# Performance work log

Hardware: AMD Instinct MI355X
Metric: run time of the kernel (lower is better)

## Reference

```python
import jax, jax.numpy as jnp
import numpy as np


@jax.custom_vjp
def binary_act(x):
    # sign forward, straight-through (clipped) backward, matching BinaryActivation
    return jnp.sign(x)

def _ba_fwd(x):
    return jnp.sign(x), x

def _ba_bwd(x, g):
    return (jnp.where((x >= -1.0) & (x <= 1.0), g, 0.0),)

binary_act.defvjp(_ba_fwd, _ba_bwd)


def conv2d(x, w, b, pad, groups):
    # x: NCHW, w: OIHW
    y = jax.lax.conv_general_dilated(
        x, w, window_strides=(1, 1), padding=[(pad, pad), (pad, pad)],
        feature_group_count=groups,
        dimension_numbers=("NCHW", "OIHW", "NCHW"))
    return y + b[None, :, None, None]


def bconv(x, w, b, pad, groups):
    # Binary_conv2d: weights and bias binarized via sign (no STE on weights in torch either)
    return conv2d(x, jnp.sign(w), jnp.sign(b), pad, groups)


def maxpool2(x):
    return jax.lax.reduce_window(x, -jnp.inf, jax.lax.max,
                                 (1, 1, 2, 2), (1, 1, 2, 2), "VALID")


def setup_inputs() -> dict:
    key = jax.random.key(0)
    ks = jax.random.split(key, 14)
    d = {}
    d["x"] = jax.random.normal(ks[0], (1024, 3, 32, 32), dtype=jnp.float32)
    # conv1: depthwise 3x3 (groups=3) then 1x1 3->128
    d["w1_dw"] = jax.random.normal(ks[1], (3, 1, 3, 3), dtype=jnp.float32) * 0.1
    d["b1_dw"] = jax.random.normal(ks[2], (3,), dtype=jnp.float32) * 0.1
    d["w1_pw"] = jax.random.normal(ks[3], (128, 3, 1, 1), dtype=jnp.float32) * 0.1
    d["b1_pw"] = jax.random.normal(ks[4], (128,), dtype=jnp.float32) * 0.1
    # conv2: depthwise 3x3 (groups=128) then 1x1 128->256
    d["w2_dw"] = jax.random.normal(ks[5], (128, 1, 3, 3), dtype=jnp.float32) * 0.1
    d["b2_dw"] = jax.random.normal(ks[6], (128,), dtype=jnp.float32) * 0.1
    d["w2_pw"] = jax.random.normal(ks[7], (256, 128, 1, 1), dtype=jnp.float32) * 0.1
    d["b2_pw"] = jax.random.normal(ks[8], (256,), dtype=jnp.float32) * 0.1
    # fc layers (full precision weights, sign applied to fc1 output only)
    d["fc1_w"] = jax.random.normal(ks[9], (1024, 256 * 8 * 8), dtype=jnp.float32) * (1.0 / np.sqrt(256 * 8 * 8))
    d["fc1_b"] = jnp.zeros((1024,), dtype=jnp.float32)
    d["fc2_w"] = jax.random.normal(ks[10], (10, 1024), dtype=jnp.float32) * (1.0 / np.sqrt(1024.0))
    d["fc2_b"] = jnp.zeros((10,), dtype=jnp.float32)
    return d


def reference(x, w1_dw, b1_dw, w1_pw, b1_pw, w2_dw, b2_dw, w2_pw, b2_pw,
              fc1_w, fc1_b, fc2_w, fc2_b):
    h = bconv(x, w1_dw, b1_dw, pad=1, groups=3)        # [B,3,32,32]
    h = bconv(h, w1_pw, b1_pw, pad=0, groups=1)        # [B,128,32,32]
    h = maxpool2(binary_act(h))                        # [B,128,16,16]
    h = bconv(h, w2_dw, b2_dw, pad=1, groups=128)      # [B,128,16,16]
    h = bconv(h, w2_pw, b2_pw, pad=0, groups=1)        # [B,256,16,16]
    h = maxpool2(binary_act(h))                        # [B,256,8,8]
    h = h.reshape(h.shape[0], -1)                      # [B,16384]
    h = binary_act(h @ fc1_w.T + fc1_b)                # [B,1024]
    return h @ fc2_w.T + fc2_b                         # [B,10]
```

## Files before the change

### kernel.cpp

```cpp
#include <hip/hip_runtime.h>


__device__ __forceinline__ int fsign(float v)  { return (v > 0.f) - (v < 0.f); }
__device__ __forceinline__ int dsign(double v) { return (v > 0.0) - (v < 0.0); }

typedef int v4i __attribute__((ext_vector_type(4)));

__device__ __forceinline__ void async16(const signed char* g, signed char* l) {
    __builtin_amdgcn_global_load_lds(
        (const __attribute__((address_space(1))) void*)g,
        (__attribute__((address_space(3))) void*)l, 16, 0, 0);
}

__global__ void k1_conv1(const float* __restrict__ x,
                         const float* __restrict__ w1dw, const float* __restrict__ b1dw,
                         const float* __restrict__ w1pw, const float* __restrict__ b1pw,
                         const float* __restrict__ w2pw, const float* __restrict__ b2pw,
                         signed char* __restrict__ pooled1T,
                         signed char* __restrict__ w2s, int* __restrict__ b2adj)
{
    __shared__ float sdw[27], sbdw[3];
    __shared__ unsigned char spidx[128];
    __shared__ __align__(16) signed char Obuf[32768];
    int t = threadIdx.x;
    if (t < 27) sdw[t] = (float)fsign(w1dw[t]);
    if (t < 3)  sbdw[t] = (float)fsign(b1dw[t]);
    if (t < 128) {
        int b0 = w1pw[t * 3 + 0] > 0.f;
        int b1 = w1pw[t * 3 + 1] > 0.f;
        int b2 = w1pw[t * 3 + 2] > 0.f;
        int b3 = b1pw[t] > 0.f;
        spidx[t] = (unsigned char)(b0 | (b1 << 1) | (b2 << 2) | (b3 << 3));
    }
    __syncthreads();

    int g  = blockIdx.x * 256 + t;
    int px = g & 15, py = (g >> 4) & 15, n = g >> 8;

    double h[3][4];
    const float* xb = x + (size_t)n * 3 * 1024;
    #pragma unroll
    for (int c = 0; c < 3; c++) {
        const float* xc = xb + c * 1024;
        #pragma unroll
        for (int dy = 0; dy < 2; dy++)
        #pragma unroll
        for (int dx = 0; dx < 2; dx++) {
            int y = 2 * py + dy, xx = 2 * px + dx;
            double acc = (double)sbdw[c];
            #pragma unroll
            for (int ky = 0; ky < 3; ky++) {
                int yy = y + ky - 1;
                if (yy < 0 || yy > 31) continue;
                #pragma unroll
                for (int kx = 0; kx < 3; kx++) {
                    int xxx = xx + kx - 1;
                    if (xxx < 0 || xxx > 31) continue;
                    acc += (double)sdw[c * 9 + ky * 3 + kx] * (double)xc[yy * 32 + xxx];
                }
            }
            h[c][dy * 2 + dx] = acc;
        }
    }

    double tv[4][4];
    #pragma unroll
    for (int q = 0; q < 4; q++) {
        double u = h[0][q] + h[1][q];
        double v = h[0][q] - h[1][q];
        tv[0][q] = v - h[2][q];
        tv[1][q] = u - h[2][q];
        tv[2][q] = v + h[2][q];
        tv[3][q] = u + h[2][q];
    }
    int mpack = 0;
    #pragma unroll
    for (int bp = 0; bp < 4; bp++) {
        int mxP = -2, mnP = 2, mxM = -2, mnM = 2;
        #pragma unroll
        for (int q = 0; q < 4; q++) {
            int sP = dsign(tv[bp][q] + 1.0);
            int sM = dsign(tv[bp][q] - 1.0);
            mxP = max(mxP, sP); mnP = min(mnP, sP);
            mxM = max(mxM, sM); mnM = min(mnM, sM);
        }
        int pat1 = 1 | (bp << 1);
        int pat0 = (~pat1) & 7;
        mpack |= (mxP + 1)   << (2 * (pat1 | 8));
        mpack |= (mxM + 1)   << (2 * pat1);
        mpack |= ((-mnM) + 1) << (2 * (pat0 | 8));
        mpack |= ((-mnP) + 1) << (2 * pat0);
    }

    signed char* orow = Obuf + t * 128;
    const int* pint = (const int*)spidx;
    for (int ob = 0; ob < 32; ob++) {
        int pw = pint[ob];
        int cur = 0;
        #pragma unroll
        for (int e = 0; e < 4; e++) {
            int pi = (pw >> (8 * e)) & 15;
            int mv = ((mpack >> (pi * 2)) & 3) - 1;
            cur |= (mv & 0xff) << (8 * e);
        }
        int ad = (((ob >> 2) ^ (t & 7)) << 4) + (ob & 3) * 4;
        *(int*)(orow + ad) = cur;
    }
    __syncthreads();

    signed char* outb = pooled1T + (size_t)blockIdx.x * 32768;
    #pragma unroll
    for (int r = 0; r < 8; r++) {
        int o = r * 4096 + t * 16;
        int pix = o >> 7, gg = (o >> 4) & 7;
        *(int4*)(outb + o) = *(const int4*)&Obuf[pix * 128 + ((gg ^ (pix & 7)) << 4)];
    }

    if (blockIdx.x == 0) {
        int o = t;
        int rs = 0;
        for (int cq = 0; cq < 32; cq++) {
            float4 w = *(const float4*)(w2pw + (size_t)o * 128 + cq * 4);
            int s0 = fsign(w.x), s1 = fsign(w.y), s2 = fsign(w.z), s3 = fsign(w.w);
            rs += s0 + s1 + s2 + s3;
            int pk = (s0 & 0xff) | ((s1 & 0xff) << 8) | ((s2 & 0xff) << 16) | ((s3 & 0xff) << 24);
            *(int*)(w2s + (size_t)o * 128 + cq * 4) = pk;
        }
        b2adj[o] = fsign(b2pw[o]) - 32 * rs;
    }
}

__global__ __launch_bounds__(256, 4) void k3_fused(
    const signed char* __restrict__ pooled1T,
    const float* __restrict__ w2dw, const float* __restrict__ b2dw,
    const signed char* __restrict__ w2s, const int* __restrict__ b2adj,
    signed char* __restrict__ hT2)
{
    __shared__ __align__(16) signed char Ps[32768];
    __shared__ __align__(16) signed char Uni[5120];
    __shared__ int sb2adj[256];

    signed char* sw4  = Uni;
    signed char* sdb2 = Uni + 1152;
    signed char* Os   = Uni;

    int t = threadIdx.x, l = t & 63, wid = t >> 6;
    int n = blockIdx.x;
    const signed char* pb = pooled1T + (size_t)n * 32768;

    #pragma unroll
    for (int it = 0; it < 8; it++) {
        int off = it * 4096 + t * 16;
        int p = off >> 7, seg = (off >> 4) & 7;
        *(int4*)&Ps[p * 128 + ((seg ^ (p & 7)) * 16)] = *(const int4*)(pb + off);
    }
    for (int i = t; i < 1152; i += 256) {
        int c = i & 127, tap = i >> 7;
        sw4[tap * 128 + c] = (signed char)fsign(w2dw[c * 9 + tap]);
    }
    if (t < 128) sdb2[t] = (signed char)(fsign(b2dw[t]) + 1);
    if (t < 256) sb2adj[t] = b2adj[t];
    __syncthreads();

    int frow = l & 15;

    v4i af[4][2];
    #pragma unroll
    for (int ks = 0; ks < 2; ks++) {
        int c0 = ks * 64 + (l >> 4) * 16;
        int cc = c0 >> 4;
        int4 w4[9];
        #pragma unroll
        for (int tap = 0; tap < 9; tap++)
            w4[tap] = *(const int4*)&sw4[tap * 128 + c0];
        int4 sdbv = *(const int4*)&sdb2[c0];

        #pragma unroll
        for (int i = 0; i < 4; i++) {
            int r = (wid * 4 + i) * 16 + frow;
            int py = r >> 5, px2 = (r >> 2) & 7, dy = (r >> 1) & 1, dx = r & 1;
            int y = 2 * py + dy, x = 2 * px2 + dx;
            int4 cnt = (int4){0, 0, 0, 0};
            #pragma unroll
            for (int ky = 0; ky < 3; ky++) {
                int yy = y + ky - 1;
                int yc = min(max(yy, 0), 15);
                #pragma unroll
                for (int kx = 0; kx < 3; kx++) {
                    int xx2 = x + kx - 1;
                    int xc = min(max(xx2, 0), 15);
                    int inb = ((yy == yc) && (xx2 == xc)) ? 0x01010101 : 0;
                    int p = yc * 16 + xc;
                    int4 v = *(const int4*)&Ps[p * 128 + ((cc ^ (p & 7)) * 16)];
                    int4 w = w4[ky * 3 + kx];
                    cnt.x += ((v.x ^ w.x) >> 1) & inb;
                    cnt.y += ((v.y ^ w.y) >> 1) & inb;
                    cnt.z += ((v.z ^ w.z) >> 1) & inb;
                    cnt.w += ((v.w ^ w.w) >> 1) & inb;
                }
            }
            int valid = (1 + (y > 0) + (y < 15)) * (1 + (x > 0) + (x < 15));
            int mb = (valid + 31) * 0x01010101;
            int4 u;
            u.x = sdbv.x + mb - (cnt.x + cnt.x);
            u.y = sdbv.y + mb - (cnt.y + cnt.y);
            u.z = sdbv.z + mb - (cnt.z + cnt.z);
            u.w = sdbv.w + mb - (cnt.w + cnt.w);
            af[i][ks] = (v4i){u.x, u.y, u.z, u.w};
        }
    }

    for (int oc = 0; oc < 4; oc++) {
        v4i acc[4][4];
        #pragma unroll
        for (int i = 0; i < 4; i++)
            #pragma unroll
            for (int jt = 0; jt < 4; jt++) acc[i][jt] = (v4i){0, 0, 0, 0};

        #pragma unroll
        for (int ks = 0; ks < 2; ks++) {
            v4i bf[4];
            #pragma unroll
            for (int jt = 0; jt < 4; jt++)
                bf[jt] = *(const v4i*)(w2s + (size_t)(oc * 64 + jt * 16 + frow) * 128
                                       + ks * 64 + (l >> 4) * 16);
            __builtin_amdgcn_s_setprio(1);
            #pragma unroll
            for (int i = 0; i < 4; i++)
                #pragma unroll
                for (int jt = 0; jt < 4; jt++)
                    acc[i][jt] = __builtin_amdgcn_mfma_i32_16x16x64_i8(af[i][ks], bf[jt], acc[i][jt], 0, 0, 0);
            __builtin_amdgcn_s_setprio(0);
        }

        __syncthreads();
        #pragma unroll
        for (int jt = 0; jt < 4; jt++) {
            int o_l = jt * 16 + frow;
            int bia = sb2adj[oc * 64 + o_l];
            #pragma unroll
            for (int i = 0; i < 4; i++) {
                int mx = -2;
                #pragma unroll
                for (int rr = 0; rr < 4; rr++) {
                    int p = acc[i][jt][rr] + bia;
                    int s = (p > 0) - (p < 0);
                    mx = s > mx ? s : mx;
                }
                int pp = (wid * 4 + i) * 4 + (l >> 4);
                Os[o_l * 80 + pp] = (signed char)mx;
            }
        }
        __syncthreads();
        *(int4*)&hT2[(size_t)n * 16384 + oc * 4096 + t * 16]
            = *(const int4*)&Os[(t >> 2) * 80 + (t & 3) * 16];
    }
}

__global__ void kprep(const float* __restrict__ fc1w, signed char* __restrict__ BL)
{
    int t = threadIdx.x;
    int b = blockIdx.x;
    int j = b >> 4, kb = b & 15;
    int k0 = kb * 1024 + t * 4;
    float4 w = *(const float4*)(fc1w + (size_t)j * 16384 + k0);
    float we[4] = {w.x, w.y, w.z, w.w};
    int out[4] = {0, 0, 0, 0};
    #pragma unroll
    for (int e = 0; e < 4; e++) {
        int q = (int)rint((double)we[e] * 4294967296.0);
        q = min(max(q, -266338304), 266338304);
        int d0 = ((q + 64) & 127) - 64; q = (q - d0) >> 7;
        int d1 = ((q + 64) & 127) - 64; q = (q - d1) >> 7;
        int d2 = ((q + 64) & 127) - 64; q = (q - d2) >> 7;
        int d3 = q;
        out[0] |= (d0 & 0xff) << (8 * e);
        out[1] |= (d1 & 0xff) << (8 * e);
        out[2] |= (d2 & 0xff) << (8 * e);
        out[3] |= (d3 & 0xff) << (8 * e);
    }
    #pragma unroll
    for (int m = 0; m < 4; m++)
        *(int*)(BL + (size_t)(j * 4 + m) * 16384 + k0) = out[m];
}

__global__ __launch_bounds__(512, 2) void k4a_fc1(
    const signed char* __restrict__ hT2, const signed char* __restrict__ BL,
    double* __restrict__ Pd)
{
    __shared__ __align__(16) signed char smem[98304];
    int t = threadIdx.x, l = t & 63, wid = t >> 6;
    int nb0 = blockIdx.y * 128, jb0 = blockIdx.x * 256;
    int kh = blockIdx.z, k0 = kh * 8192;
    int ksw = wid >> 2;
    int wn0 = ((wid >> 1) & 1) * 64, wj0 = (wid & 1) * 128;

    int srow = l >> 3;
    int sseg = ((l & 7) ^ srow) * 16;
    const signed char* gA = hT2 + (size_t)(nb0 + wid * 16 + srow) * 16384 + k0 + sseg;
    const signed char* gB = BL  + (size_t)(jb0 + wid * 32 + srow) * 16384 + k0 + sseg;

    v4i acc[4][8];
    #pragma unroll
    for (int i = 0; i < 4; i++)
        #pragma unroll
        for (int q = 0; q < 8; q++) acc[i][q] = (v4i){0, 0, 0, 0};

    {
        signed char* As = smem;
        signed char* Bs = smem + 16384;
        #pragma unroll
        for (int c = 0; c < 2; c++)
            async16(gA + (size_t)c * 8 * 16384, As + (wid * 16 + c * 8) * 128);
        #pragma unroll
        for (int c = 0; c < 4; c++)
            async16(gB + (size_t)c * 8 * 16384, Bs + (wid * 32 + c * 8) * 128);
    }

    int sw = (((ksw * 4) + (l >> 4)) ^ (l & 7)) * 16;

    for (int it = 0; it < 64; it++) {
        __syncthreads();
        if (it + 1 < 64) {
            int kt = (it + 1) * 128;
            signed char* As = smem + ((it + 1) & 1) * 49152;
            signed char* Bs = As + 16384;
            #pragma unroll
            for (int c = 0; c < 2; c++)
                async16(gA + (size_t)c * 8 * 16384 + kt, As + (wid * 16 + c * 8) * 128);
            #pragma unroll
            for (int c = 0; c < 4; c++)
                async16(gB + (size_t)c * 8 * 16384 + kt, Bs + (wid * 32 + c * 8) * 128);
        }
        const signed char* As = smem + (it & 1) * 49152;
        const signed char* Bs = As + 16384;
        v4i af[4], bf[8];
        #pragma unroll
        for (int i = 0; i < 4; i++)
            af[i] = *(const v4i*)&As[(wn0 + i * 16 + (l & 15)) * 128 + sw];
        #pragma unroll
        for (int q = 0; q < 8; q++)
            bf[q] = *(const v4i*)&Bs[(wj0 + q * 16 + (l & 15)) * 128 + sw];
        #pragma unroll
        for (int i = 0; i < 4; i++)
            #pragma unroll
            for (int q = 0; q < 8; q++)
                acc[i][q] = __builtin_amdgcn_mfma_i32_16x16x64_i8(af[i], bf[q], acc[i][q], 0, 0, 0);
    }

    __syncthreads();
    int* S = (int*)smem;
    #pragma unroll
    for (int h = 0; h < 2; h++) {
        if (h) __syncthreads();
        if (ksw == 0 && wn0 == h * 64) {
            #pragma unroll
            for (int i = 0; i < 4; i++)
                #pragma unroll
                for (int q = 0; q < 8; q++)
                    #pragma unroll
                    for (int rr = 0; rr < 4; rr++)
                        S[(i * 16 + (l >> 4) * 4 + rr) * 256 + (wj0 + q * 16 + (l & 15))]
                            = acc[i][q][rr];
        }
        __syncthreads();
        if (ksw == 1 && wn0 == h * 64) {
            #pragma unroll
            for (int i = 0; i < 4; i++)
                #pragma unroll
                for (int q = 0; q < 8; q++)
                    #pragma unroll
                    for (int rr = 0; rr < 4; rr++)
                        S[(i * 16 + (l >> 4) * 4 + rr) * 256 + (wj0 + q * 16 + (l & 15))]
                            += acc[i][q][rr];
        }
        __syncthreads();
        #pragma unroll
        for (int e = 0; e < 8; e++) {
            int idx = t * 8 + e;
            int n_l = idx >> 6, j_l = idx & 63;
            int4 s = *(const int4*)&S[n_l * 256 + j_l * 4];
            double val = (double)s.x + 128.0 * (double)s.y
                       + 16384.0 * (double)s.z + 2097152.0 * (double)s.w;
            Pd[(size_t)kh * 1048576 + (size_t)(nb0 + h * 64 + n_l) * 1024
               + blockIdx.x * 64 + j_l] = val;
        }
    }
}

__global__ __launch_bounds__(256) void k45_comb_fc2(
    const double* __restrict__ Pd, const float* __restrict__ fc1b,
    const float* __restrict__ fc2w, const float* __restrict__ fc2b,
    float* __restrict__ out)
{
    __shared__ double sj[1024];
    __shared__ double pw[4][10];
    int t = threadIdx.x, n = blockIdx.x;
    const double SCALE = 1.0 / 4294967296.0;

    #pragma unroll
    for (int rep = 0; rep < 4; rep++) {
        int j = rep * 256 + t;
        double v = Pd[(size_t)n * 1024 + j] + Pd[1048576 + (size_t)n * 1024 + j];
        double p = v * SCALE + (double)fc1b[j];
        sj[j] = (double)((p > 0.0) - (p < 0.0));
    }
    __syncthreads();

    int j0 = t * 4;
    double s0 = sj[j0], s1 = sj[j0 + 1], s2 = sj[j0 + 2], s3 = sj[j0 + 3];
    double acc[10];
    #pragma unroll
    for (int m = 0; m < 10; m++) {
        float4 w = *(const float4*)(fc2w + (size_t)m * 1024 + j0);
        acc[m] = s0 * (double)w.x + s1 * (double)w.y + s2 * (double)w.z + s3 * (double)w.w;
    }
    #pragma unroll
    for (int off = 32; off > 0; off >>= 1)
        #pragma unroll
        for (int m = 0; m < 10; m++)
            acc[m] += __shfl_down(acc[m], off);
    if ((t & 63) == 0)
        #pragma unroll
        for (int m = 0; m < 10; m++) pw[t >> 6][m] = acc[m];
    __syncthreads();
    if (t < 10)
        out[n * 10 + t] = (float)(pw[0][t] + pw[1][t] + pw[2][t] + pw[3][t] + (double)fc2b[t]);
}

__global__ __launch_bounds__(512) void k4_fc1_mfma(
    const signed char* __restrict__ hT2, const signed char* __restrict__ BL,
    const float* __restrict__ fc1b, signed char* __restrict__ hs)
{
    __shared__ __align__(16) signed char smem[65536];
    int t = threadIdx.x, l = t & 63, wid = t >> 6;
    int nb0 = blockIdx.y * 128, jb0 = blockIdx.x * 128;
    int wn0 = (wid >> 1) * 32;
    int wj0 = (wid & 1) * 64;

    int srow = l >> 3;
    int sseg = ((l & 7) ^ srow) * 16;
    const signed char* gA = hT2 + (size_t)(nb0 + wid * 16 + srow) * 16384 + sseg;
    const signed char* gB = BL  + (size_t)(jb0 + wid * 16 + srow) * 16384 + sseg;

    v4i acc[2][4];
    #pragma unroll
    for (int i = 0; i < 2; i++)
        #pragma unroll
        for (int q = 0; q < 4; q++) acc[i][q] = (v4i){0, 0, 0, 0};

    {
        signed char* As = smem;
        signed char* Bs = smem + 16384;
        #pragma unroll
        for (int i = 0; i < 2; i++) {
            async16(gA + (size_t)i * 8 * 16384, As + (wid * 16 + i * 8) * 128);
            async16(gB + (size_t)i * 8 * 16384, Bs + (wid * 16 + i * 8) * 128);
        }
    }

    for (int it = 0; it < 128; it++) {
        __syncthreads();
        if (it + 1 < 128) {
            int kt = (it + 1) * 128;
            signed char* As = smem + ((it + 1) & 1) * 32768;
            signed char* Bs = As + 16384;
            #pragma unroll
            for (int i = 0; i < 2; i++) {
                async16(gA + (size_t)i * 8 * 16384 + kt, As + (wid * 16 + i * 8) * 128);
                async16(gB + (size_t)i * 8 * 16384 + kt, Bs + (wid * 16 + i * 8) * 128);
            }
        }
        const signed char* As = smem + (it & 1) * 32768;
        const signed char* Bs = As + 16384;
        #pragma unroll
        for (int ks = 0; ks < 2; ks++) {
            int sw = (((ks * 4) + (l >> 4)) ^ (l & 7)) * 16;
            v4i af[2], bf[4];
            #pragma unroll
            for (int i = 0; i < 2; i++)
                af[i] = *(const v4i*)&As[(wn0 + i * 16 + (l & 15)) * 128 + sw];
            #pragma unroll
            for (int q = 0; q < 4; q++)
                bf[q] = *(const v4i*)&Bs[(wj0 + q * 16 + (l & 15)) * 128 + sw];
            #pragma unroll
            for (int i = 0; i < 2; i++)
                #pragma unroll
                for (int q = 0; q < 4; q++)
                    acc[i][q] = __builtin_amdgcn_mfma_i32_16x16x64_i8(af[i], bf[q], acc[i][q], 0, 0, 0);
        }
    }

    __syncthreads();
    int* S = (int*)smem;
    #pragma unroll
    for (int i = 0; i < 2; i++)
        #pragma unroll
        for (int q = 0; q < 4; q++)
            #pragma unroll
            for (int rr = 0; rr < 4; rr++) {
                int n_l  = wn0 + i * 16 + (l >> 4) * 4 + rr;
                int jm_l = wj0 + q * 16 + (l & 15);
                S[n_l * 128 + jm_l] = acc[i][q][rr];
            }
    __syncthreads();

    const double SCALE = 1.0 / 4294967296.0;
    #pragma unroll
    for (int i = 0; i < 8; i++) {
        int idx = t * 8 + i;
        int n_l = idx >> 5, j_l = idx & 31;
        int4 s = *(const int4*)&S[n_l * 128 + j_l * 4];
        double val = (double)s.x + 128.0 * (double)s.y
                   + 16384.0 * (double)s.z + 2097152.0 * (double)s.w;
        int j = blockIdx.x * 32 + j_l;
        double p = val * SCALE + (double)fc1b[j];
        hs[(size_t)(nb0 + n_l) * 1024 + j] = (signed char)((p > 0.0) - (p < 0.0));
    }
}

__global__ void k5_fc2(const signed char* __restrict__ hs,
                       const float* __restrict__ fc2w, const float* __restrict__ fc2b,
                       float* __restrict__ out)
{
    int idx = blockIdx.x * 64 + threadIdx.x;
    if (idx >= 10240) return;
    int n = idx / 10, m = idx - n * 10;
    const signed char* hr = hs + (size_t)n * 1024;
    const float* wr = fc2w + (size_t)m * 1024;
    double acc = (double)fc2b[m];
    for (int jb = 0; jb < 1024; jb += 16) {
        int4 hv = *(const int4*)(hr + jb);
        int wd[4] = {hv.x, hv.y, hv.z, hv.w};
        #pragma unroll
        for (int u = 0; u < 4; u++)
            #pragma unroll
            for (int e = 0; e < 4; e++)
                acc += (double)(signed char)(wd[u] >> (8 * e)) * (double)wr[jb + u * 4 + e];
    }
    out[idx] = (float)acc;
}

extern "C" void kernel_launch(void* const* d_in, const int* in_sizes, int n_in,
                              void* d_out, int out_size, void* d_ws, size_t ws_size,
                              hipStream_t stream)
{
    const float* x    = (const float*)d_in[0];
    const float* w1dw = (const float*)d_in[1];
    const float* b1dw = (const float*)d_in[2];
    const float* w1pw = (const float*)d_in[3];
    const float* b1pw = (const float*)d_in[4];
    const float* w2dw = (const float*)d_in[5];
    const float* b2dw = (const float*)d_in[6];
    const float* w2pw = (const float*)d_in[7];
    const float* b2pw = (const float*)d_in[8];
    const float* fc1w = (const float*)d_in[9];
    const float* fc1b = (const float*)d_in[10];
    const float* fc2w = (const float*)d_in[11];
    const float* fc2b = (const float*)d_in[12];
    float* out = (float*)d_out;

    char* ws = (char*)d_ws;
    signed char* pooled1T = (signed char*)(ws);
    signed char* hT2      = (signed char*)(ws + 67108864);
    signed char* w2s      = (signed char*)(ws + 83886080);
    int*         b2adj    = (int*)(ws + 83886080 + 32768);
    signed char* BL       = (signed char*)(ws);
    signed char* hs       = (signed char*)(ws + 83886080);
    double*      Pd       = (double*)(ws + 84934656);
    bool split = ws_size >= (size_t)84934656 + 16777216;

    hipLaunchKernelGGL(k1_conv1,  dim3(1024),  dim3(256), 0, stream,
                       x, w1dw, b1dw, w1pw, b1pw, w2pw, b2pw, pooled1T, w2s, b2adj);
    hipLaunchKernelGGL(k3_fused,  dim3(1024),  dim3(256), 0, stream,
                       pooled1T, w2dw, b2dw, w2s, b2adj, hT2);
    hipLaunchKernelGGL(kprep,     dim3(16384), dim3(256), 0, stream,
                       fc1w, BL);
    if (split) {
        hipLaunchKernelGGL(k4a_fc1,      dim3(16, 8, 2), dim3(512), 0, stream,
                           hT2, BL, Pd);
        hipLaunchKernelGGL(k45_comb_fc2, dim3(1024),     dim3(256), 0, stream,
                           Pd, fc1b, fc2w, fc2b, out);
    } else {
        hipLaunchKernelGGL(k4_fc1_mfma, dim3(32, 8), dim3(512), 0, stream,
                           hT2, BL, fc1b, hs);
        hipLaunchKernelGGL(k5_fc2,      dim3(160),   dim3(64),  0, stream,
                           hs, fc2w, fc2b, out);
    }
}
```

Before: 326.7 us.

## Fuse conv1 stage into conv2 kernel, keeping pooled activations in LDS

Merges the first-layer depthwise/pointwise/sign/pool computation into the second conv kernel, so each block writes its pooled 16x16x128 int8 tile straight into shared memory instead of writing to and re-reading a 32 MB global buffer. The w2 sign-packing moves to a tiny separate prep kernel, and the hs workspace offset is shifted to avoid overlapping w2s. This removes a global round-trip and a launch boundary, but the fused kernel now carries the double-precision conv1 work, which adds register pressure under the 4-blocks-per-CU launch bound.

```diff
diff --git a/kernel.cpp b/kernel.cpp
--- a/kernel.cpp
+++ b/kernel.cpp
@@ -12,17 +12,42 @@
         (__attribute__((address_space(3))) void*)l, 16, 0, 0);
 }
 
-__global__ void k1_conv1(const float* __restrict__ x,
-                         const float* __restrict__ w1dw, const float* __restrict__ b1dw,
-                         const float* __restrict__ w1pw, const float* __restrict__ b1pw,
-                         const float* __restrict__ w2pw, const float* __restrict__ b2pw,
-                         signed char* __restrict__ pooled1T,
-                         signed char* __restrict__ w2s, int* __restrict__ b2adj)
-{
+__global__ void kprep2(const float* __restrict__ w2pw, const float* __restrict__ b2pw,
+                       signed char* __restrict__ w2s, int* __restrict__ b2adj)
+{
+    int o = blockIdx.x * 64 + threadIdx.x;
+    int rs = 0;
+    for (int cq = 0; cq < 32; cq++) {
+        float4 w = *(const float4*)(w2pw + (size_t)o * 128 + cq * 4);
+        int s0 = fsign(w.x), s1 = fsign(w.y), s2 = fsign(w.z), s3 = fsign(w.w);
+        rs += s0 + s1 + s2 + s3;
+        int pk = (s0 & 0xff) | ((s1 & 0xff) << 8) | ((s2 & 0xff) << 16) | ((s3 & 0xff) << 24);
+        *(int*)(w2s + (size_t)o * 128 + cq * 4) = pk;
+    }
+    b2adj[o] = fsign(b2pw[o]) - 32 * rs;
+}
+
+__global__ __launch_bounds__(256, 4) void k13_fused(
+    const float* __restrict__ x,
+    const float* __restrict__ w1dw, const float* __restrict__ b1dw,
+    const float* __restrict__ w1pw, const float* __restrict__ b1pw,
+    const float* __restrict__ w2dw, const float* __restrict__ b2dw,
+    const signed char* __restrict__ w2s, const int* __restrict__ b2adj,
+    signed char* __restrict__ hT2)
+{
+    __shared__ __align__(16) signed char Ps[32768];
+    __shared__ __align__(16) signed char Uni[5120];
+    __shared__ int sb2adj[256];
     __shared__ float sdw[27], sbdw[3];
     __shared__ unsigned char spidx[128];
-    __shared__ __align__(16) signed char Obuf[32768];
-    int t = threadIdx.x;
+
+    signed char* sw4  = Uni;
+    signed char* sdb2 = Uni + 1152;
+    signed char* Os   = Uni;
+
+    int t = threadIdx.x, l = t & 63, wid = t >> 6;
+    int n = blockIdx.x;
+
     if (t < 27) sdw[t] = (float)fsign(w1dw[t]);
     if (t < 3)  sbdw[t] = (float)fsign(b1dw[t]);
     if (t < 128) {
@@ -32,134 +57,86 @@
         int b3 = b1pw[t] > 0.f;
         spidx[t] = (unsigned char)(b0 | (b1 << 1) | (b2 << 2) | (b3 << 3));
     }
-    __syncthreads();
-
-    int g  = blockIdx.x * 256 + t;
-    int px = g & 15, py = (g >> 4) & 15, n = g >> 8;
-
-    double h[3][4];
-    const float* xb = x + (size_t)n * 3 * 1024;
-    #pragma unroll
-    for (int c = 0; c < 3; c++) {
-        const float* xc = xb + c * 1024;
-        #pragma unroll
-        for (int dy = 0; dy < 2; dy++)
-        #pragma unroll
-        for (int dx = 0; dx < 2; dx++) {
-            int y = 2 * py + dy, xx = 2 * px + dx;
-            double acc = (double)sbdw[c];
-            #pragma unroll
-            for (int ky = 0; ky < 3; ky++) {
-                int yy = y + ky - 1;
-                if (yy < 0 || yy > 31) continue;
-                #pragma unroll
-                for (int kx = 0; kx < 3; kx++) {
-                    int xxx = xx + kx - 1;
-                    if (xxx < 0 || xxx > 31) continue;
-                    acc += (double)sdw[c * 9 + ky * 3 + kx] * (double)xc[yy * 32 + xxx];
-                }
-            }
-            h[c][dy * 2 + dx] = acc;
-        }
-    }
-
-    double tv[4][4];
-    #pragma unroll
-    for (int q = 0; q < 4; q++) {
-        double u = h[0][q] + h[1][q];
-        double v = h[0][q] - h[1][q];
-        tv[0][q] = v - h[2][q];
-        tv[1][q] = u - h[2][q];
-        tv[2][q] = v + h[2][q];
-        tv[3][q] = u + h[2][q];
-    }
-    int mpack = 0;
-    #pragma unroll
-    for (int bp = 0; bp < 4; bp++) {
-        int mxP = -2, mnP = 2, mxM = -2, mnM = 2;
-        #pragma unroll
-        for (int q = 0; q < 4; q++) {
-            int sP = dsign(tv[bp][q] + 1.0);
-            int sM = dsign(tv[bp][q] - 1.0);
-            mxP = max(mxP, sP); mnP = min(mnP, sP);
-            mxM = max(mxM, sM); mnM = min(mnM, sM);
-        }
-        int pat1 = 1 | (bp << 1);
-        int pat0 = (~pat1) & 7;
-        mpack |= (mxP + 1)   << (2 * (pat1 | 8));
-        mpack |= (mxM + 1)   << (2 * pat1);
-        mpack |= ((-mnM) + 1) << (2 * (pat0 | 8));
-        mpack |= ((-mnP) + 1) << (2 * pat0);
-    }
-
-    signed char* orow = Obuf + t * 128;
-    const int* pint = (const int*)spidx;
-    for (int ob = 0; ob < 32; ob++) {
-        int pw = pint[ob];
-        int cur = 0;
-        #pragma unroll
-        for (int e = 0; e < 4; e++) {
-            int pi = (pw >> (8 * e)) & 15;
-            int mv = ((mpack >> (pi * 2)) & 3) - 1;
-            cur |= (mv & 0xff) << (8 * e);
-        }
-        int ad = (((ob >> 2) ^ (t & 7)) << 4) + (ob & 3) * 4;
-        *(int*)(orow + ad) = cur;
-    }
-    __syncthreads();
-
-    signed char* outb = pooled1T + (size_t)blockIdx.x * 32768;
-    #pragma unroll
-    for (int r = 0; r < 8; r++) {
-        int o = r * 4096 + t * 16;
-        int pix = o >> 7, gg = (o >> 4) & 7;
-        *(int4*)(outb + o) = *(const int4*)&Obuf[pix * 128 + ((gg ^ (pix & 7)) << 4)];
-    }
-
-    if (blockIdx.x == 0) {
-        int o = t;
-        int rs = 0;
-        for (int cq = 0; cq < 32; cq++) {
-            float4 w = *(const float4*)(w2pw + (size_t)o * 128 + cq * 4);
-            int s0 = fsign(w.x), s1 = fsign(w.y), s2 = fsign(w.z), s3 = fsign(w.w);
-            rs += s0 + s1 + s2 + s3;
-            int pk = (s0 & 0xff) | ((s1 & 0xff) << 8) | ((s2 & 0xff) << 16) | ((s3 & 0xff) << 24);
-            *(int*)(w2s + (size_t)o * 128 + cq * 4) = pk;
-        }
-        b2adj[o] = fsign(b2pw[o]) - 32 * rs;
-    }
-}
-
-__global__ __launch_bounds__(256, 4) void k3_fused(
-    const signed char* __restrict__ pooled1T,
-    const float* __restrict__ w2dw, const float* __restrict__ b2dw,
-    const signed char* __restrict__ w2s, const int* __restrict__ b2adj,
-    signed char* __restrict__ hT2)
-{
-    __shared__ __align__(16) signed char Ps[32768];
-    __shared__ __align__(16) signed char Uni[5120];
-    __shared__ int sb2adj[256];
-
-    signed char* sw4  = Uni;
-    signed char* sdb2 = Uni + 1152;
-    signed char* Os   = Uni;
-
-    int t = threadIdx.x, l = t & 63, wid = t >> 6;
-    int n = blockIdx.x;
-    const signed char* pb = pooled1T + (size_t)n * 32768;
-
-    #pragma unroll
-    for (int it = 0; it < 8; it++) {
-        int off = it * 4096 + t * 16;
-        int p = off >> 7, seg = (off >> 4) & 7;
-        *(int4*)&Ps[p * 128 + ((seg ^ (p & 7)) * 16)] = *(const int4*)(pb + off);
-    }
     for (int i = t; i < 1152; i += 256) {
         int c = i & 127, tap = i >> 7;
         sw4[tap * 128 + c] = (signed char)fsign(w2dw[c * 9 + tap]);
     }
     if (t < 128) sdb2[t] = (signed char)(fsign(b2dw[t]) + 1);
-    if (t < 256) sb2adj[t] = b2adj[t];
+    sb2adj[t] = b2adj[t];
+    __syncthreads();
+
+    {
+        int px = t & 15, py = t >> 4;
+        double h[3][4];
+        const float* xb = x + (size_t)n * 3 * 1024;
+        #pragma unroll
+        for (int c = 0; c < 3; c++) {
+            const float* xc = xb + c * 1024;
+            #pragma unroll
+            for (int dy = 0; dy < 2; dy++)
+            #pragma unroll
+            for (int dx = 0; dx < 2; dx++) {
+                int y = 2 * py + dy, xx = 2 * px + dx;
+                double acc = (double)sbdw[c];
+                #pragma unroll
+                for (int ky = 0; ky < 3; ky++) {
+                    int yy = y + ky - 1;
+                    if (yy < 0 || yy > 31) continue;
+                    #pragma unroll
+                    for (int kx = 0; kx < 3; kx++) {
+                        int xxx = xx + kx - 1;
+                        if (xxx < 0 || xxx > 31) continue;
+                        acc += (double)sdw[c * 9 + ky * 3 + kx] * (double)xc[yy * 32 + xxx];
+                    }
+                }
+                h[c][dy * 2 + dx] = acc;
+            }
+        }
+
+        double tv[4][4];
+        #pragma unroll
+        for (int q = 0; q < 4; q++) {
+            double u = h[0][q] + h[1][q];
+            double v = h[0][q] - h[1][q];
+            tv[0][q] = v - h[2][q];
+            tv[1][q] = u - h[2][q];
+            tv[2][q] = v + h[2][q];
+            tv[3][q] = u + h[2][q];
+        }
+        int mpack = 0;
+        #pragma unroll
+        for (int bp = 0; bp < 4; bp++) {
+            int mxP = -2, mnP = 2, mxM = -2, mnM = 2;
+            #pragma unroll
+            for (int q = 0; q < 4; q++) {
+                int sP = dsign(tv[bp][q] + 1.0);
+                int sM = dsign(tv[bp][q] - 1.0);
+                mxP = max(mxP, sP); mnP = min(mnP, sP);
+                mxM = max(mxM, sM); mnM = min(mnM, sM);
+            }
+            int pat1 = 1 | (bp << 1);
+            int pat0 = (~pat1) & 7;
+            mpack |= (mxP + 1)   << (2 * (pat1 | 8));
+            mpack |= (mxM + 1)   << (2 * pat1);
+            mpack |= ((-mnM) + 1) << (2 * (pat0 | 8));
+            mpack |= ((-mnP) + 1) << (2 * pat0);
+        }
+
+        signed char* prow = Ps + t * 128;
+        const int* pint = (const int*)spidx;
+        for (int ob = 0; ob < 32; ob++) {
+            int pw = pint[ob];
+            int cur = 0;
+            #pragma unroll
+            for (int e = 0; e < 4; e++) {
+                int pi = (pw >> (8 * e)) & 15;
+                int mv = ((mpack >> (pi * 2)) & 3) - 1;
+                cur |= (mv & 0xff) << (8 * e);
+            }
+            int ad = (((ob >> 2) ^ (t & 7)) << 4) + (ob & 3) * 4;
+            *(int*)(prow + ad) = cur;
+        }
+    }
     __syncthreads();
 
     int frow = l & 15;
@@ -179,7 +156,7 @@
         for (int i = 0; i < 4; i++) {
             int r = (wid * 4 + i) * 16 + frow;
             int py = r >> 5, px2 = (r >> 2) & 7, dy = (r >> 1) & 1, dx = r & 1;
-            int y = 2 * py + dy, x = 2 * px2 + dx;
+            int y = 2 * py + dy, xq = 2 * px2 + dx;
             int4 cnt = (int4){0, 0, 0, 0};
             #pragma unroll
             for (int ky = 0; ky < 3; ky++) {
@@ -187,7 +164,7 @@
                 int yc = min(max(yy, 0), 15);
                 #pragma unroll
                 for (int kx = 0; kx < 3; kx++) {
-                    int xx2 = x + kx - 1;
+                    int xx2 = xq + kx - 1;
                     int xc = min(max(xx2, 0), 15);
                     int inb = ((yy == yc) && (xx2 == xc)) ? 0x01010101 : 0;
                     int p = yc * 16 + xc;
@@ -199,7 +176,7 @@
                     cnt.w += ((v.w ^ w.w) >> 1) & inb;
                 }
             }
-            int valid = (1 + (y > 0) + (y < 15)) * (1 + (x > 0) + (x < 15));
+            int valid = (1 + (y > 0) + (y < 15)) * (1 + (xq > 0) + (xq < 15));
             int mb = (valid + 31) * 0x01010101;
             int4 u;
             u.x = sdbv.x + mb - (cnt.x + cnt.x);
@@ -561,19 +538,18 @@
     float* out = (float*)d_out;
 
     char* ws = (char*)d_ws;
-    signed char* pooled1T = (signed char*)(ws);
     signed char* hT2      = (signed char*)(ws + 67108864);
     signed char* w2s      = (signed char*)(ws + 83886080);
     int*         b2adj    = (int*)(ws + 83886080 + 32768);
     signed char* BL       = (signed char*)(ws);
-    signed char* hs       = (signed char*)(ws + 83886080);
+    signed char* hs       = (signed char*)(ws + 83886080 + 1048576);
     double*      Pd       = (double*)(ws + 84934656);
     bool split = ws_size >= (size_t)84934656 + 16777216;
 
-    hipLaunchKernelGGL(k1_conv1,  dim3(1024),  dim3(256), 0, stream,
-                       x, w1dw, b1dw, w1pw, b1pw, w2pw, b2pw, pooled1T, w2s, b2adj);
-    hipLaunchKernelGGL(k3_fused,  dim3(1024),  dim3(256), 0, stream,
-                       pooled1T, w2dw, b2dw, w2s, b2adj, hT2);
+    hipLaunchKernelGGL(kprep2,    dim3(4),     dim3(64),  0, stream,
+                       w2pw, b2pw, w2s, b2adj);
+    hipLaunchKernelGGL(k13_fused, dim3(1024),  dim3(256), 0, stream,
+                       x, w1dw, b1dw, w1pw, b1pw, w2dw, b2dw, w2s, b2adj, hT2);
     hipLaunchKernelGGL(kprep,     dim3(16384), dim3(256), 0, stream,
                        fc1w, BL);
     if (split) {
```

After: 324.6 us. About the same (-0.6%).
